# Kernel optimization log

Measured on AMD Instinct MI355X. Metric: run time of the kernel, lower is better.

Reference implementation:

```python
import jax, jax.numpy as jnp
import numpy as np

B, H, W, T = 2, 48, 48, 48
DIM, NH, KS = 384, 6, 3
HD = DIM // NH
K3 = KS ** 3  # 27 local neighbors


def setup_inputs() -> dict:
    key = jax.random.key(0)
    k1, k2, k3 = jax.random.split(key, 3)
    q = jax.random.normal(k1, (B, H, W, T, DIM), dtype=jnp.float32)
    k = jax.random.normal(k2, (B, H, W, T, DIM), dtype=jnp.float32)
    rpb = jax.random.normal(k3, (NH, KS, KS, KS), dtype=jnp.float32) * 0.02
    # fixed displacement vectors: meshgrid of [-1, 0, 1]^3, 'ij' indexing -> (27, 3)
    vec = jnp.arange(-(KS // 2), KS // 2 + 1, dtype=jnp.float32)
    grid = jnp.stack(jnp.meshgrid(vec, vec, vec, indexing='ij'), axis=-1)
    v = grid.reshape(K3, 3)
    return {"q": q, "k": k, "rpb": rpb, "v": v}


def reference(q, k, rpb, v):
    scale = HD ** (-0.5)
    # (B,H,W,T,NH,HD), pre-scaled queries
    qh = q.reshape(B, H, W, T, NH, HD) * scale
    kh = k.reshape(B, H, W, T, NH, HD)
    pdr = KS // 2
    k_pad = jnp.pad(kh, ((0, 0), (pdr, pdr), (pdr, pdr), (pdr, pdr), (0, 0), (0, 0)))
    # local QK logits: for each of the 27 offsets, dot q with the shifted k.
    # Loop is over a fixed tiny neighborhood (27), not over data dims, and
    # avoids materializing a [27,B,H,W,T,C] gather tensor.
    logits = []
    for di in range(KS):
        for dj in range(KS):
            for dl in range(KS):
                ks = k_pad[:, di:di + H, dj:dj + W, dl:dl + T]  # (B,H,W,T,NH,HD)
                logits.append(jnp.einsum('bxyznd,bxyznd->bxyzn', qh, ks))
    attn = jnp.stack(logits, axis=-1)  # (B,H,W,T,NH,27)
    attn = attn + rpb.reshape(NH, K3)  # relative position bias
    attn = jax.nn.softmax(attn, axis=-1)
    # weighted sum of fixed displacement vectors: (B,H,W,T,NH,3)
    x = jnp.einsum('bxyzno,oc->bxyznc', attn, v)
    x = x.reshape(B, H, W, T, NH * 3)
    return x.transpose(0, 4, 1, 2, 3)  # (B, NH*3, H, W, T)
```

## Files before the change

kernel.cpp:

```cpp
#include <hip/hip_runtime.h>

namespace {

constexpr int DIM = 384;
constexpr int NH  = 6;
constexpr float L2E    = 1.44269504088896f;
constexpr float SCALE2 = 0.125f * L2E;

constexpr int TILES  = 12 * 12 * 12;
constexpr int NBLK   = 2 * TILES;

typedef _Float16 half8  __attribute__((ext_vector_type(8)));
typedef _Float16 half2v __attribute__((ext_vector_type(2)));
typedef __fp16   fp16x2 __attribute__((ext_vector_type(2)));
typedef float    floatx4 __attribute__((ext_vector_type(4)));
typedef unsigned uintx4 __attribute__((ext_vector_type(4)));

__device__ __forceinline__ half2v pk(float a, float b) {
    fp16x2 t = __builtin_amdgcn_cvt_pkrtz(a, b);
    return __builtin_bit_cast(half2v, t);
}

__global__ __launch_bounds__(256, 2)
void natten_tbl(const float* __restrict__ q, const float* __restrict__ k,
                const float* __restrict__ rpb, float* __restrict__ out)
{
    __shared__ _Float16 k_lds[224 * 64];
    __shared__ unsigned tbl_lds[7 * 256];
    __shared__ float    rpbL[NH * 32];

    const int bid0 = blockIdx.x;
    const int bid  = (bid0 & 7) * (NBLK / 8) + (bid0 >> 3);
    const int tile = bid % TILES;
    const int b    = bid / TILES;
    const int tz = (tile % 12) * 4;
    const int ty = ((tile / 12) % 12) * 4;
    const int tx = (tile / 144) * 4;

    const int tid = threadIdx.x;
    const int w = tid >> 6, lane = tid & 63;
    const int lrow = lane & 15, lgrp = lane >> 4;
    char* kl = (char*)k_lds;

    const float* kbb = k + (size_t)b * 110592 * DIM;
    const int col0 = tid >> 3, ch = tid & 7;
    char* dst = kl + col0 * 128 + ((ch * 16) ^ ((col0 & 7) << 4));
    int      koff[7];
    unsigned um[7];
    {
        int cx = 0, cy = col0 / 6, cz = col0 - (col0 / 6) * 6;
        #pragma unroll
        for (int it = 0; it < 7; ++it) {
            const int gx = tx + cx - 1, gy = ty + cy - 1, gz = tz + cz - 1;
            const bool v = ((unsigned)gx < 48u) && ((unsigned)gy < 48u) &&
                           ((unsigned)gz < 48u);
            const int cgx = min(max(gx, 0), 47);
            const int cgy = min(max(gy, 0), 47);
            const int cgz = min(max(gz, 0), 47);
            koff[it] = ((cgx * 48 + cgy) * 48 + cgz) * DIM + ch * 8;
            um[it] = v ? 0xFFFFFFFFu : 0u;
            cz += 2; if (cz >= 6) { cz -= 6; cy += 1; }
            cy += 5; if (cy >= 6) { cy -= 6; cx += 1; }
        }
    }
    const int qyo = lrow >> 2, qzo = lrow & 3;
    const float* qrow = q + ((size_t)b * 110592
        + (size_t)(((tx + w) * 48 + (ty + qyo)) * 48 + (tz + qzo))) * DIM + lgrp * 8;

    float4 P0[7], P1[7], QP[4];
    auto issue = [&](int n) {
        const float* kb = kbb + n * 64;
        #pragma unroll
        for (int it = 0; it < 7; ++it) {
            P0[it] = *(const float4*)(kb + koff[it]);
            P1[it] = *(const float4*)(kb + koff[it] + 4);
        }
        const float* qp = qrow + n * 64;
        QP[0] = ((const float4*)qp)[0];
        QP[1] = ((const float4*)qp)[1];
        QP[2] = ((const float4*)(qp + 32))[0];
        QP[3] = ((const float4*)(qp + 32))[1];
    };
    issue(0);

    #pragma unroll
    for (int i = 0; i < 7; ++i) {
        const int u  = 16 * i + ((tid >> 6) << 2) + (tid & 3);
        const int lr = (tid >> 2) & 15;
        unsigned val = 124u | 0x01010100u;
        if (u < 108) {
            const int rx = u / 36, rem = u - rx * 36;
            const int ry = rem / 6, rz = rem - ry * 6;
            const int dj = ry - (lr >> 2), dl = rz - (lr & 3);
            if ((unsigned)dj <= 2u && (unsigned)dl <= 2u)
                val = (unsigned)(((rx * 9 + dj * 3 + dl) << 2)
                      | (rx << 8) | (dj << 16) | (dl << 24));
        }
        tbl_lds[i * 256 + tid] = val;
    }
    if (tid < NH * 32) {
        const int n = tid >> 5, o = tid & 31;
        rpbL[tid] = (o < 27) ? rpb[n * 27 + o] * L2E : -1e30f;
    }
    __syncthreads();

    uintx4 tr[7];
    #pragma unroll
    for (int j = 0; j < 7; ++j)
        tr[j] = *(const uintx4*)&tbl_lds[j * 256 + lgrp * 64 + lrow * 4];

    const int cbase = w * 36 + lrow;
    const int xm2 = (cbase & 7) << 4;
    const char* bpA = kl + cbase * 128 + ((lgrp * 16) ^ xm2);
    const char* bpB = kl + cbase * 128 + ((lgrp * 16 + 64) ^ xm2);

    for (int n = 0; n < NH; ++n) {
        if (n) __builtin_amdgcn_s_barrier();

        #pragma unroll
        for (int it = 0; it < 7; ++it) {
            half8 h;
            ((half2v*)&h)[0] = pk(P0[it].x, P0[it].y);
            ((half2v*)&h)[1] = pk(P0[it].z, P0[it].w);
            ((half2v*)&h)[2] = pk(P1[it].x, P1[it].y);
            ((half2v*)&h)[3] = pk(P1[it].z, P1[it].w);
            uintx4 hv = __builtin_bit_cast(uintx4, h);
            const uintx4 m4 = {um[it], um[it], um[it], um[it]};
            hv &= m4;
            *(uintx4*)(dst + it * 4096) = hv;
        }
        half8 a0, a1;
        ((half2v*)&a0)[0] = pk(QP[0].x, QP[0].y);
        ((half2v*)&a0)[1] = pk(QP[0].z, QP[0].w);
        ((half2v*)&a0)[2] = pk(QP[1].x, QP[1].y);
        ((half2v*)&a0)[3] = pk(QP[1].z, QP[1].w);
        ((half2v*)&a1)[0] = pk(QP[2].x, QP[2].y);
        ((half2v*)&a1)[1] = pk(QP[2].z, QP[2].w);
        ((half2v*)&a1)[2] = pk(QP[3].x, QP[3].y);
        ((half2v*)&a1)[3] = pk(QP[3].z, QP[3].w);

        if (n + 1 < NH) issue(n + 1);
        __builtin_amdgcn_sched_barrier(0);
        asm volatile("s_waitcnt lgkmcnt(0)" ::: "memory");
        __builtin_amdgcn_sched_barrier(0);
        __builtin_amdgcn_s_barrier();

        floatx4 acc[7];
        #pragma unroll
        for (int j = 0; j < 7; ++j) {
            const half8 b0 = *(const half8*)(bpA + j * 2048);
            const half8 b1 = *(const half8*)(bpB + j * 2048);
            floatx4 c = {0.f, 0.f, 0.f, 0.f};
            c = __builtin_amdgcn_mfma_f32_16x16x32_f16(b0, a0, c, 0, 0, 0);
            c = __builtin_amdgcn_mfma_f32_16x16x32_f16(b1, a1, c, 0, 0, 0);
            acc[j] = c;
        }

        const char* rpbLn = (const char*)rpbL + n * 128;
        float den = 0.f, sx = 0.f, sy = 0.f, sz = 0.f;
        #pragma unroll
        for (int j = 0; j < 7; ++j) {
            #pragma unroll
            for (int r = 0; r < 4; ++r) {
                const unsigned t = tr[j][r];
                const float bias = *(const float*)(rpbLn + (t & 124u));
                const float e = __builtin_amdgcn_exp2f(fmaf(acc[j][r], SCALE2, bias));
                den += e;
                sx = fmaf(e, (float)((t >> 8) & 255u), sx);
                sy = fmaf(e, (float)((t >> 16) & 255u), sy);
                sz = fmaf(e, (float)(t >> 24), sz);
            }
        }
        den += __shfl_xor(den, 16); den += __shfl_xor(den, 32);
        sx  += __shfl_xor(sx, 16);  sx  += __shfl_xor(sx, 32);
        sy  += __shfl_xor(sy, 16);  sy  += __shfl_xor(sy, 32);
        sz  += __shfl_xor(sz, 16);  sz  += __shfl_xor(sz, 32);

        if (lgrp < 3) {
            const float s = (lgrp == 0) ? sx : (lgrp == 1 ? sy : sz);
            const float res = s / den - 1.0f;
            out[((size_t)(b * 18 + n * 3 + lgrp) * 48 + (tx + w)) * 2304
                + (size_t)(ty + qyo) * 48 + (tz + qzo)] = res;
        }
    }
}

}

extern "C" void kernel_launch(void* const* d_in, const int* in_sizes, int n_in,
                              void* d_out, int out_size, void* d_ws, size_t ws_size,
                              hipStream_t stream)
{
    (void)in_sizes; (void)n_in; (void)d_ws; (void)ws_size; (void)out_size;
    const float* q   = (const float*)d_in[0];
    const float* k   = (const float*)d_in[1];
    const float* rpb = (const float*)d_in[2];
    float* out = (float*)d_out;

    natten_tbl<<<dim3(NBLK), dim3(256), 0, stream>>>(q, k, rpb, out);
}
```

Before: 221.5 us.

## Split heads across blocks instead of looping heads inside each block

```diff
diff --git a/kernel.cpp b/kernel.cpp
--- a/kernel.cpp
+++ b/kernel.cpp
@@ -7,8 +7,8 @@
 constexpr float L2E    = 1.44269504088896f;
 constexpr float SCALE2 = 0.125f * L2E;
 
-constexpr int TILES  = 12 * 12 * 12;
-constexpr int NBLK   = 2 * TILES;
+constexpr int TILES = 12 * 12 * 12;
+constexpr int NBLK  = 2 * NH * TILES;
 
 typedef _Float16 half8  __attribute__((ext_vector_type(8)));
 typedef _Float16 half2v __attribute__((ext_vector_type(2)));
@@ -21,18 +21,32 @@
     return __builtin_bit_cast(half2v, t);
 }
 
-__global__ __launch_bounds__(256, 2)
-void natten_tbl(const float* __restrict__ q, const float* __restrict__ k,
+__device__ __forceinline__ uintx4 cvt_mask(const floatx4& u0, const floatx4& u1,
+                                           unsigned m) {
+    half8 h;
+    ((half2v*)&h)[0] = pk(u0[0], u0[1]);
+    ((half2v*)&h)[1] = pk(u0[2], u0[3]);
+    ((half2v*)&h)[2] = pk(u1[0], u1[1]);
+    ((half2v*)&h)[3] = pk(u1[2], u1[3]);
+    uintx4 hv = __builtin_bit_cast(uintx4, h);
+    const uintx4 m4 = {m, m, m, m};
+    return hv & m4;
+}
+
+__global__ __launch_bounds__(256)
+__attribute__((amdgpu_waves_per_eu(2, 4)))
+void natten_reg(const float* __restrict__ q, const float* __restrict__ k,
                 const float* __restrict__ rpb, float* __restrict__ out)
 {
     __shared__ _Float16 k_lds[224 * 64];
     __shared__ unsigned tbl_lds[7 * 256];
-    __shared__ float    rpbL[NH * 32];
+    __shared__ float    rpbL[32];
 
     const int bid0 = blockIdx.x;
     const int bid  = (bid0 & 7) * (NBLK / 8) + (bid0 >> 3);
-    const int tile = bid % TILES;
-    const int b    = bid / TILES;
+    const int n    = bid % NH;
+    const int tile = (bid / NH) % TILES;
+    const int b    = bid / (NH * TILES);
     const int tz = (tile % 12) * 4;
     const int ty = ((tile / 12) % 12) * 4;
     const int tx = (tile / 144) * 4;
@@ -42,46 +56,7 @@
     const int lrow = lane & 15, lgrp = lane >> 4;
     char* kl = (char*)k_lds;
 
-    const float* kbb = k + (size_t)b * 110592 * DIM;
-    const int col0 = tid >> 3, ch = tid & 7;
-    char* dst = kl + col0 * 128 + ((ch * 16) ^ ((col0 & 7) << 4));
-    int      koff[7];
-    unsigned um[7];
-    {
-        int cx = 0, cy = col0 / 6, cz = col0 - (col0 / 6) * 6;
-        #pragma unroll
-        for (int it = 0; it < 7; ++it) {
-            const int gx = tx + cx - 1, gy = ty + cy - 1, gz = tz + cz - 1;
-            const bool v = ((unsigned)gx < 48u) && ((unsigned)gy < 48u) &&
-                           ((unsigned)gz < 48u);
-            const int cgx = min(max(gx, 0), 47);
-            const int cgy = min(max(gy, 0), 47);
-            const int cgz = min(max(gz, 0), 47);
-            koff[it] = ((cgx * 48 + cgy) * 48 + cgz) * DIM + ch * 8;
-            um[it] = v ? 0xFFFFFFFFu : 0u;
-            cz += 2; if (cz >= 6) { cz -= 6; cy += 1; }
-            cy += 5; if (cy >= 6) { cy -= 6; cx += 1; }
-        }
-    }
-    const int qyo = lrow >> 2, qzo = lrow & 3;
-    const float* qrow = q + ((size_t)b * 110592
-        + (size_t)(((tx + w) * 48 + (ty + qyo)) * 48 + (tz + qzo))) * DIM + lgrp * 8;
-
-    float4 P0[7], P1[7], QP[4];
-    auto issue = [&](int n) {
-        const float* kb = kbb + n * 64;
-        #pragma unroll
-        for (int it = 0; it < 7; ++it) {
-            P0[it] = *(const float4*)(kb + koff[it]);
-            P1[it] = *(const float4*)(kb + koff[it] + 4);
-        }
-        const float* qp = qrow + n * 64;
-        QP[0] = ((const float4*)qp)[0];
-        QP[1] = ((const float4*)qp)[1];
-        QP[2] = ((const float4*)(qp + 32))[0];
-        QP[3] = ((const float4*)(qp + 32))[1];
-    };
-    issue(0);
+    if (tid < 32) rpbL[tid] = (tid < 27) ? rpb[n * 27 + tid] * L2E : -1e30f;
 
     #pragma unroll
     for (int i = 0; i < 7; ++i) {
@@ -98,10 +73,71 @@
         }
         tbl_lds[i * 256 + tid] = val;
     }
-    if (tid < NH * 32) {
-        const int n = tid >> 5, o = tid & 31;
-        rpbL[tid] = (o < 27) ? rpb[n * 27 + o] * L2E : -1e30f;
-    }
+
+    const float* kb = k + (size_t)b * 110592 * DIM + n * 64;
+    const int col0 = tid >> 3, ch = tid & 7;
+    char* dst = kl + col0 * 128 + ((ch * 16) ^ ((col0 & 7) << 4));
+    const float* ks[7];
+    unsigned     um[7];
+    {
+        int cx = 0, cy = col0 / 6, cz = col0 - (col0 / 6) * 6;
+        #pragma unroll
+        for (int it = 0; it < 7; ++it) {
+            const int gx = tx + cx - 1, gy = ty + cy - 1, gz = tz + cz - 1;
+            const bool v = ((unsigned)gx < 48u) && ((unsigned)gy < 48u) &&
+                           ((unsigned)gz < 48u);
+            const int cgx = min(max(gx, 0), 47);
+            const int cgy = min(max(gy, 0), 47);
+            const int cgz = min(max(gz, 0), 47);
+            ks[it] = kb + ((cgx * 48 + cgy) * 48 + cgz) * DIM + ch * 8;
+            um[it] = v ? 0xFFFFFFFFu : 0u;
+            cz += 2; if (cz >= 6) { cz -= 6; cy += 1; }
+            cy += 5; if (cy >= 6) { cy -= 6; cx += 1; }
+        }
+    }
+    const int qyo = lrow >> 2, qzo = lrow & 3;
+    const float* qp = q + ((size_t)b * 110592
+        + (size_t)(((tx + w) * 48 + (ty + qyo)) * 48 + (tz + qzo))) * DIM
+        + n * 64 + lgrp * 8;
+
+    __syncthreads();
+
+    floatx4 F0[7], F1[7], Q0, Q1, Q2, Q3;
+    #pragma unroll
+    for (int it = 0; it < 7; ++it) {
+        asm volatile(
+            "global_load_dwordx4 %0, %2, off\n\t"
+            "global_load_dwordx4 %1, %2, off offset:16"
+            : "=&v"(F0[it]), "=&v"(F1[it]) : "v"(ks[it]) : "memory");
+    }
+    asm volatile(
+        "global_load_dwordx4 %0, %4, off\n\t"
+        "global_load_dwordx4 %1, %4, off offset:16\n\t"
+        "global_load_dwordx4 %2, %4, off offset:128\n\t"
+        "global_load_dwordx4 %3, %4, off offset:144"
+        : "=&v"(Q0), "=&v"(Q1), "=&v"(Q2), "=&v"(Q3) : "v"(qp) : "memory");
+
+    asm volatile("s_waitcnt vmcnt(8)"
+        : "+v"(F0[0]), "+v"(F0[1]), "+v"(F0[2]), "+v"(F0[3]), "+v"(F0[4]),
+          "+v"(F1[0]), "+v"(F1[1]), "+v"(F1[2]), "+v"(F1[3]), "+v"(F1[4]) ::);
+    __builtin_amdgcn_sched_barrier(0);
+    #pragma unroll
+    for (int it = 0; it < 5; ++it)
+        *(uintx4*)(dst + it * 4096) = cvt_mask(F0[it], F1[it], um[it]);
+
+    asm volatile("s_waitcnt vmcnt(0)"
+        : "+v"(F0[5]), "+v"(F0[6]), "+v"(F1[5]), "+v"(F1[6]),
+          "+v"(Q0), "+v"(Q1), "+v"(Q2), "+v"(Q3) ::);
+    __builtin_amdgcn_sched_barrier(0);
+    #pragma unroll
+    for (int it = 5; it < 7; ++it)
+        *(uintx4*)(dst + it * 4096) = cvt_mask(F0[it], F1[it], um[it]);
+
+    half8 a0, a1;
+    ((half2v*)&a0)[0] = pk(Q0[0], Q0[1]); ((half2v*)&a0)[1] = pk(Q0[2], Q0[3]);
+    ((half2v*)&a0)[2] = pk(Q1[0], Q1[1]); ((half2v*)&a0)[3] = pk(Q1[2], Q1[3]);
+    ((half2v*)&a1)[0] = pk(Q2[0], Q2[1]); ((half2v*)&a1)[1] = pk(Q2[2], Q2[3]);
+    ((half2v*)&a1)[2] = pk(Q3[0], Q3[1]); ((half2v*)&a1)[3] = pk(Q3[2], Q3[3]);
     __syncthreads();
 
     uintx4 tr[7];
@@ -113,75 +149,41 @@
     const int xm2 = (cbase & 7) << 4;
     const char* bpA = kl + cbase * 128 + ((lgrp * 16) ^ xm2);
     const char* bpB = kl + cbase * 128 + ((lgrp * 16 + 64) ^ xm2);
-
-    for (int n = 0; n < NH; ++n) {
-        if (n) __builtin_amdgcn_s_barrier();
-
+    floatx4 acc[7];
+    #pragma unroll
+    for (int j = 0; j < 7; ++j) {
+        const half8 b0 = *(const half8*)(bpA + j * 2048);
+        const half8 b1 = *(const half8*)(bpB + j * 2048);
+        floatx4 c = {0.f, 0.f, 0.f, 0.f};
+        c = __builtin_amdgcn_mfma_f32_16x16x32_f16(b0, a0, c, 0, 0, 0);
+        c = __builtin_amdgcn_mfma_f32_16x16x32_f16(b1, a1, c, 0, 0, 0);
+        acc[j] = c;
+    }
+
+    float den = 0.f, sx = 0.f, sy = 0.f, sz = 0.f;
+    #pragma unroll
+    for (int j = 0; j < 7; ++j) {
         #pragma unroll
-        for (int it = 0; it < 7; ++it) {
-            half8 h;
-            ((half2v*)&h)[0] = pk(P0[it].x, P0[it].y);
-            ((half2v*)&h)[1] = pk(P0[it].z, P0[it].w);
-            ((half2v*)&h)[2] = pk(P1[it].x, P1[it].y);
-            ((half2v*)&h)[3] = pk(P1[it].z, P1[it].w);
-            uintx4 hv = __builtin_bit_cast(uintx4, h);
-            const uintx4 m4 = {um[it], um[it], um[it], um[it]};
-            hv &= m4;
-            *(uintx4*)(dst + it * 4096) = hv;
+        for (int r = 0; r < 4; ++r) {
+            const unsigned t = tr[j][r];
+            const float bias = *(const float*)((const char*)rpbL + (t & 124u));
+            const float e = __builtin_amdgcn_exp2f(fmaf(acc[j][r], SCALE2, bias));
+            den += e;
+            sx = fmaf(e, (float)((t >> 8) & 255u), sx);
+            sy = fmaf(e, (float)((t >> 16) & 255u), sy);
+            sz = fmaf(e, (float)(t >> 24), sz);
         }
-        half8 a0, a1;
-        ((half2v*)&a0)[0] = pk(QP[0].x, QP[0].y);
-        ((half2v*)&a0)[1] = pk(QP[0].z, QP[0].w);
-        ((half2v*)&a0)[2] = pk(QP[1].x, QP[1].y);
-        ((half2v*)&a0)[3] = pk(QP[1].z, QP[1].w);
-        ((half2v*)&a1)[0] = pk(QP[2].x, QP[2].y);
-        ((half2v*)&a1)[1] = pk(QP[2].z, QP[2].w);
-        ((half2v*)&a1)[2] = pk(QP[3].x, QP[3].y);
-        ((half2v*)&a1)[3] = pk(QP[3].z, QP[3].w);
-
-        if (n + 1 < NH) issue(n + 1);
-        __builtin_amdgcn_sched_barrier(0);
-        asm volatile("s_waitcnt lgkmcnt(0)" ::: "memory");
-        __builtin_amdgcn_sched_barrier(0);
-        __builtin_amdgcn_s_barrier();
-
-        floatx4 acc[7];
-        #pragma unroll
-        for (int j = 0; j < 7; ++j) {
-            const half8 b0 = *(const half8*)(bpA + j * 2048);
-            const half8 b1 = *(const half8*)(bpB + j * 2048);
-            floatx4 c = {0.f, 0.f, 0.f, 0.f};
-            c = __builtin_amdgcn_mfma_f32_16x16x32_f16(b0, a0, c, 0, 0, 0);
-            c = __builtin_amdgcn_mfma_f32_16x16x32_f16(b1, a1, c, 0, 0, 0);
-            acc[j] = c;
-        }
-
-        const char* rpbLn = (const char*)rpbL + n * 128;
-        float den = 0.f, sx = 0.f, sy = 0.f, sz = 0.f;
-        #pragma unroll
-        for (int j = 0; j < 7; ++j) {
-            #pragma unroll
-            for (int r = 0; r < 4; ++r) {
-                const unsigned t = tr[j][r];
-                const float bias = *(const float*)(rpbLn + (t & 124u));
-                const float e = __builtin_amdgcn_exp2f(fmaf(acc[j][r], SCALE2, bias));
-                den += e;
-                sx = fmaf(e, (float)((t >> 8) & 255u), sx);
-                sy = fmaf(e, (float)((t >> 16) & 255u), sy);
-                sz = fmaf(e, (float)(t >> 24), sz);
-            }
-        }
-        den += __shfl_xor(den, 16); den += __shfl_xor(den, 32);
-        sx  += __shfl_xor(sx, 16);  sx  += __shfl_xor(sx, 32);
-        sy  += __shfl_xor(sy, 16);  sy  += __shfl_xor(sy, 32);
-        sz  += __shfl_xor(sz, 16);  sz  += __shfl_xor(sz, 32);
-
-        if (lgrp < 3) {
-            const float s = (lgrp == 0) ? sx : (lgrp == 1 ? sy : sz);
-            const float res = s / den - 1.0f;
-            out[((size_t)(b * 18 + n * 3 + lgrp) * 48 + (tx + w)) * 2304
-                + (size_t)(ty + qyo) * 48 + (tz + qzo)] = res;
-        }
+    }
+    den += __shfl_xor(den, 16); den += __shfl_xor(den, 32);
+    sx  += __shfl_xor(sx, 16);  sx  += __shfl_xor(sx, 32);
+    sy  += __shfl_xor(sy, 16);  sy  += __shfl_xor(sy, 32);
+    sz  += __shfl_xor(sz, 16);  sz  += __shfl_xor(sz, 32);
+
+    if (lgrp < 3) {
+        const float s = (lgrp == 0) ? sx : (lgrp == 1 ? sy : sz);
+        const float res = s / den - 1.0f;
+        out[((size_t)(b * 18 + n * 3 + lgrp) * 48 + (tx + w)) * 2304
+            + (size_t)(ty + qyo) * 48 + (tz + qzo)] = res;
     }
 }
 
@@ -197,5 +199,5 @@
     const float* rpb = (const float*)d_in[2];
     float* out = (float*)d_out;
 
-    natten_tbl<<<dim3(NBLK), dim3(256), 0, stream>>>(q, k, rpb, out);
-}
+    natten_reg<<<dim3(NBLK), dim3(256), 0, stream>>>(q, k, rpb, out);
+}
```

New measurement: 211.1 us. 4.7% less time.
